# Kernel tuning notes

Measured on AMD Instinct MI355X. Metric: run time of the kernel, lower is better.

## Reference

```python
import jax, jax.numpy as jnp
import numpy as np

B, S, E, H, Dh, R, L = 32, 512, 512, 8, 64, 3, 2
NI, NS = 10000, 1000
SCALE = float(1.0 / np.sqrt(Dh))
NEG = -1000000000.0


def _tensor_attn(q, kv, Wq, bq, Wk, bk, Wv, bv, Wg, bg, Wtq, btq, Wtk, btk, core, mask):
    # q, kv: [B,S,E]
    Q = q @ Wq + bq
    K = kv @ Wk + bk
    V = kv @ Wv + bv
    # per-query global bias computed from full key projection: [B,S,H] -> [B,H,S,1]
    glo = jnp.transpose(K @ Wg + bg, (0, 2, 1))[..., None]
    Qh = Q.reshape(B, S, H, Dh).transpose(0, 2, 1, 3)  # [B,H,S,Dh]
    Kh = K.reshape(B, S, H, Dh).transpose(0, 2, 1, 3)
    Vh = V.reshape(B, S, H, Dh).transpose(0, 2, 1, 3)
    scores = jnp.einsum('bhqd,bhkd->bhqk', Qh, Kh)  # [B,H,S,S]
    # low-rank bilinear tensor-core term; note it depends only on position s
    qt = Qh @ Wtq + btq  # [B,H,S,R]
    kt = Kh @ Wtk + btk  # [B,H,S,R]
    ts = jnp.einsum('bhsi,ij,bhsj->bhs', qt, core, kt)  # [B,H,S]
    scores = (scores + glo + ts[..., None]) * SCALE
    scores = jnp.where(mask, NEG, scores)
    p = jax.nn.softmax(scores, axis=-1)
    out = jnp.einsum('bhqk,bhkd->bhqd', p, Vh)
    return out.transpose(0, 2, 1, 3).reshape(B, S, E)


def setup_inputs() -> dict:
    key = jax.random.key(0)
    ks = jax.random.split(key, 24)
    f = lambda k, shp, s=0.02: (jax.random.normal(k, shp, dtype=jnp.float32) * s)
    inp = {}
    inp['item_inputs'] = jax.random.randint(ks[0], (B, S), 0, NI)
    inp['skill_inputs'] = jax.random.randint(ks[1], (B, S), 0, NS)
    inp['label_inputs'] = jax.random.randint(ks[2], (B, S), 0, 2)
    inp['item_ids'] = jax.random.randint(ks[3], (B, S), 0, NI)
    inp['skill_ids'] = jax.random.randint(ks[4], (B, S), 0, NS)
    inp['item_emb'] = f(ks[5], (NI + 1, E // 2), 1.0).at[0].set(0.0)  # padding_idx=0
    inp['skill_emb'] = f(ks[6], (NS + 1, E // 2), 1.0).at[0].set(0.0)
    inp['W_in'] = f(ks[7], (2 * E, E))
    inp['b_in'] = jnp.zeros((E,), jnp.float32)
    inp['Wq'] = f(ks[8], (L, E, E))
    inp['bq'] = jnp.zeros((L, E), jnp.float32)
    inp['Wk'] = f(ks[9], (L, E, E))
    inp['bk'] = jnp.zeros((L, E), jnp.float32)
    inp['Wv'] = f(ks[10], (L, E, E))
    inp['bv'] = jnp.zeros((L, E), jnp.float32)
    inp['Wg'] = f(ks[11], (L, E, H))
    inp['bg'] = jnp.zeros((L, H), jnp.float32)
    inp['Wtq'] = f(ks[12], (L, Dh, R), 0.1)
    inp['btq'] = jnp.zeros((L, R), jnp.float32)
    inp['Wtk'] = f(ks[13], (L, Dh, R), 0.1)
    inp['btk'] = jnp.zeros((L, R), jnp.float32)
    inp['core'] = f(ks[14], (L, R, R), 0.5)
    inp['W_out'] = f(ks[15], (E, 1))
    inp['b_out'] = jnp.zeros((1,), jnp.float32)
    return inp


def reference(item_inputs, skill_inputs, label_inputs, item_ids, skill_ids,
              item_emb, skill_emb, W_in, b_in, Wq, bq, Wk, bk, Wv, bv,
              Wg, bg, Wtq, btq, Wtk, btk, core, W_out, b_out):
    # get_inputs
    ie = item_emb[item_inputs]    # [B,S,E/2]
    se = skill_emb[skill_inputs]
    lab = label_inputs[..., None].astype(jnp.float32)
    half = jnp.concatenate([ie, se], axis=-1)  # [B,S,E]
    inputs = jnp.concatenate([half * lab, half * (1.0 - lab)], axis=-1)  # [B,S,2E]
    x = jax.nn.relu(inputs @ W_in + b_in)  # [B,S,E]
    # query
    query = jnp.concatenate([item_emb[item_ids], skill_emb[skill_ids]], axis=-1)
    mask = jnp.triu(jnp.ones((1, 1, S, S), dtype=bool), k=1)
    out = _tensor_attn(query, x, Wq[0], bq[0], Wk[0], bk[0], Wv[0], bv[0],
                       Wg[0], bg[0], Wtq[0], btq[0], Wtk[0], btk[0], core[0], mask)
    for l in range(1, L):
        res = _tensor_attn(query, out, Wq[l], bq[l], Wk[l], bk[l], Wv[l], bv[l],
                           Wg[l], bg[l], Wtq[l], btq[l], Wtk[l], btk[l], core[l], mask)
        out = out + jax.nn.relu(res)
    return out @ W_out + b_out  # [B,S,1]
```

## Files before the change

kernel.cpp:

```cpp
#include <hip/hip_runtime.h>
#include <stdint.h>


typedef short short8v __attribute__((ext_vector_type(8)));
typedef float f32x4 __attribute__((ext_vector_type(4)));

__device__ __forceinline__ float bf2f(unsigned short u) {
  union { unsigned int i; float f; } c;
  c.i = ((unsigned int)u) << 16;
  return c.f;
}
__device__ __forceinline__ unsigned short f2bf(float f) {
  union { float f; unsigned int i; } c;
  c.f = f;
  unsigned int u = c.i + 0x7FFFu + ((c.i >> 16) & 1u);
  return (unsigned short)(u >> 16);
}

__device__ __forceinline__ void g2l16(const void* g, void* l) {
  __builtin_amdgcn_global_load_lds(
      (const __attribute__((address_space(1))) unsigned int*)g,
      (__attribute__((address_space(3))) unsigned int*)l, 16, 0, 0);
}

struct WPtrs {
  const float* s[7];
  unsigned short* d[7];
};
__global__ __launch_bounds__(256) void transpose_all_k(WPtrs p) {
  __shared__ float t[32][33];
  int by = blockIdx.y;
  int mi, r0t;
  if (by < 32) { mi = 0; r0t = by; }
  else { mi = 1 + ((by - 32) >> 4); r0t = (by - 32) & 15; }
  const float* in = p.s[mi];
  unsigned short* out = p.d[mi];
  int R = (mi == 0) ? 1024 : 512;
  const int C = 512;
  int c0 = blockIdx.x * 32, r0 = r0t * 32;
  int lr = threadIdx.x >> 5, lc = threadIdx.x & 31;
#pragma unroll
  for (int i = 0; i < 4; ++i) {
    int r = lr + i * 8;
    t[r][lc] = in[(size_t)(r0 + r) * C + (c0 + lc)];
  }
  __syncthreads();
#pragma unroll
  for (int i = 0; i < 4; ++i) {
    int r = lr + i * 8;
    out[(size_t)(c0 + r) * R + (r0 + lc)] = f2bf(t[lc][r]);
  }
}

__global__ __launch_bounds__(256) void build_inputs_k(
    const int* __restrict__ item_in, const int* __restrict__ skill_in,
    const int* __restrict__ label_in, const int* __restrict__ item_id,
    const int* __restrict__ skill_id, const float* __restrict__ iemb,
    const float* __restrict__ semb, unsigned short* __restrict__ INP,
    unsigned short* __restrict__ QRY) {
  int w = threadIdx.x >> 6, lane = threadIdx.x & 63;
  int row = blockIdx.x * 4 + w;
  int ii = item_in[row], si = skill_in[row], lb = label_in[row];
  int iq = item_id[row], sq = skill_id[row];
  int c = lane * 16;
  int k = c & 511;
  const float* src = (k < 256) ? (iemb + (size_t)ii * 256 + k)
                               : (semb + (size_t)si * 256 + (k - 256));
  bool keep = ((lb == 1) == (c < 512));
  union { unsigned short u[16]; int4 v[2]; } o;
#pragma unroll
  for (int i = 0; i < 16; ++i) o.u[i] = keep ? f2bf(src[i]) : 0;
  *(int4*)(INP + (size_t)row * 1024 + c) = o.v[0];
  *(int4*)(INP + (size_t)row * 1024 + c + 8) = o.v[1];
  int qc = lane * 8;
  const float* qs = (qc < 256) ? (iemb + (size_t)iq * 256 + qc)
                               : (semb + (size_t)sq * 256 + (qc - 256));
  union { unsigned short u[8]; int4 v; } q;
#pragma unroll
  for (int i = 0; i < 8; ++i) q.u[i] = f2bf(qs[i]);
  *(int4*)(QRY + (size_t)row * 512 + qc) = q.v;
}

#define CT_LD 132
template <int MT>
__global__ __launch_bounds__(256, 4) void gemm_bt_k(
    const unsigned short* __restrict__ A, const unsigned short* __restrict__ Bt,
    unsigned short* __restrict__ C, int K, int ldc,
    const float* __restrict__ biasA, const float* __restrict__ biasB,
    int nsplit, float scale, int do_relu) {
  constexpr int NT = (MT == 128) ? 4 : 2;
  constexpr int US = ((MT * 64 + 128 * 64) > (MT * 132)) ? (MT * 64 + 128 * 64) : (MT * 132);
  __shared__ __align__(16) unsigned short uS[US];
  unsigned short* sA = uS;
  unsigned short* sB = uS + MT * 64;
  unsigned short* Ct = uS;
  int mb = blockIdx.x, nb = blockIdx.y;
  int tid = threadIdx.x;
  int w = tid >> 6, lane = tid & 63, l16 = lane & 15, quad = lane >> 4;
  int wm = (MT == 128) ? (w & 1) : 0;
  int wn = (MT == 128) ? (w >> 1) : w;
  f32x4 acc[4][NT];
#pragma unroll
  for (int i = 0; i < 4; ++i)
#pragma unroll
    for (int jn = 0; jn < NT; ++jn) acc[i][jn] = (f32x4){0.f, 0.f, 0.f, 0.f};

  for (int k0 = 0; k0 < K; k0 += 64) {
    __syncthreads();
#pragma unroll
    for (int jj = 0; jj < MT / 32; ++jj) {
      int c = jj * 256 + tid;
      int row = c >> 3, kc = c & 7;
      int src = kc ^ (row & 7);
      g2l16(A + (size_t)(mb * MT + row) * K + k0 + src * 8, sA + (size_t)c * 8);
    }
#pragma unroll
    for (int jj = 0; jj < 4; ++jj) {
      int c = jj * 256 + tid;
      int row = c >> 3, kc = c & 7;
      int src = kc ^ (row & 7);
      g2l16(Bt + (size_t)(nb * 128 + row) * K + k0 + src * 8, sB + (size_t)c * 8);
    }
    __syncthreads();
#pragma unroll
    for (int kk = 0; kk < 2; ++kk) {
      short8v aF[4], bF[NT];
#pragma unroll
      for (int mt = 0; mt < 4; ++mt) {
        int r = wm * 64 + mt * 16 + l16;
        aF[mt] = *(const short8v*)(sA + r * 64 + (((kk * 4 + quad) ^ (r & 7)) << 3));
      }
#pragma unroll
      for (int nt = 0; nt < NT; ++nt) {
        int r = wn * (16 * NT) + nt * 16 + l16;
        bF[nt] = *(const short8v*)(sB + r * 64 + (((kk * 4 + quad) ^ (r & 7)) << 3));
      }
#pragma unroll
      for (int mt = 0; mt < 4; ++mt)
#pragma unroll
        for (int nt = 0; nt < NT; ++nt)
          acc[mt][nt] =
              __builtin_amdgcn_mfma_f32_16x16x32_bf16(aF[mt], bF[nt], acc[mt][nt], 0, 0, 0);
    }
  }
  __syncthreads();
#pragma unroll
  for (int mt = 0; mt < 4; ++mt)
#pragma unroll
    for (int nt = 0; nt < NT; ++nt) {
      int col = wn * (16 * NT) + nt * 16 + l16;
      int gcol = nb * 128 + col;
      float bs = (gcol < nsplit) ? biasA[gcol] : biasB[gcol - nsplit];
#pragma unroll
      for (int r = 0; r < 4; ++r) {
        int row = wm * 64 + mt * 16 + quad * 4 + r;
        float v = (acc[mt][nt][r] + bs) * scale;
        if (do_relu) v = fmaxf(v, 0.f);
        Ct[row * CT_LD + col] = f2bf(v);
      }
    }
  __syncthreads();
#pragma unroll
  for (int it = 0; it < MT / 16; ++it) {
    int row = it * 16 + (tid >> 4);
    int col8 = (tid & 15) * 8;
    *(int4*)(C + (size_t)(mb * MT + row) * ldc + nb * 128 + col8) =
        *(const int4*)(Ct + row * CT_LD + col8);
  }
}

#define VP_LD 264
__global__ __launch_bounds__(256) void vperm_k(const unsigned short* __restrict__ KVb,
                                               unsigned short* __restrict__ VT) {
  __shared__ __align__(16) unsigned short stg[64 * VP_LD];
  int kt = blockIdx.x, half = blockIdx.y, b = blockIdx.z;
  int t = threadIdx.x;
#pragma unroll
  for (int i = 0; i < 8; ++i) {
    int ch = i * 256 + t;
    int kp = ch >> 5, c = ch & 31;
    *(int4*)(stg + kp * VP_LD + c * 8) =
        *(const int4*)(KVb + (size_t)(b * 512 + kt * 64 + kp) * 1024 + 512 + half * 256 + c * 8);
  }
  __syncthreads();
#pragma unroll
  for (int i = 0; i < 8; ++i) {
    int ch = i * 256 + t;
    int d = ch >> 3, cc = ch & 7;
    union { unsigned short u[8]; int4 v; } o;
#pragma unroll
    for (int s = 0; s < 8; ++s) {
      int kp = ((cc >> 2) << 5) | ((s >> 2) << 4) | ((cc & 3) << 2) | (s & 3);
      o.u[s] = stg[kp * VP_LD + d];
    }
    *(int4*)(VT + (size_t)(b * 512 + half * 256 + d) * 512 + kt * 64 + cc * 8) = o.v;
  }
}

__global__ __launch_bounds__(256, 4) void attn_k(const unsigned short* __restrict__ Qb,
                                                 const unsigned short* __restrict__ KVb,
                                                 const unsigned short* __restrict__ VT,
                                                 unsigned short* __restrict__ Out) {
  __shared__ __align__(16) unsigned short sK[64 * 64];
  __shared__ __align__(16) unsigned short sV[64 * 64];
  int tid = threadIdx.x;
  int w = tid >> 6, lane = tid & 63;
  int l16 = lane & 15, quad = lane >> 4;
  int bh = blockIdx.x;
  int b = bh >> 3, h = bh & 7;
  int jb = 7 - (int)blockIdx.y;
  int qb = jb * 64 + w * 16;
  f32x4 zf = {0.f, 0.f, 0.f, 0.f};
  short8v onesF;
#pragma unroll
  for (int i = 0; i < 8; ++i) onesF[i] = (short)0x3F80;

  short8v qF[2];
#pragma unroll
  for (int hf = 0; hf < 2; ++hf)
    qF[hf] = *(const short8v*)(Qb + (size_t)(b * 512 + qb + l16) * 512 + h * 64 + hf * 32 +
                               quad * 8);

  f32x4 O[4], RS = zf;
#pragma unroll
  for (int dt = 0; dt < 4; ++dt) O[dt] = zf;

  const unsigned short* Kg = KVb + (size_t)(b * 512) * 1024 + h * 64;
  const unsigned short* Vg = VT + (size_t)(bh * 64) * 512;

  for (int kt = 0; kt <= jb; ++kt) {
    __syncthreads();
#pragma unroll
    for (int jj = 0; jj < 2; ++jj) {
      int c = jj * 256 + tid;
      int row = c >> 3, kc = c & 7, src = kc ^ (row & 7);
      g2l16(Kg + (size_t)(kt * 64 + row) * 1024 + src * 8, sK + c * 8);
    }
#pragma unroll
    for (int jj = 0; jj < 2; ++jj) {
      int c = jj * 256 + tid;
      int row = c >> 3, kc = c & 7, src = kc ^ (row & 7);
      g2l16(Vg + (size_t)row * 512 + kt * 64 + src * 8, sV + c * 8);
    }
    __syncthreads();
#pragma unroll
    for (int kp = 0; kp < 2; ++kp) {
      int kb32 = kt * 64 + kp * 32;
      if (kb32 > qb) continue;
      short8v kC[2][2], vC[4];
#pragma unroll
      for (int v = 0; v < 2; ++v) {
        int r = kp * 32 + v * 16 + l16;
#pragma unroll
        for (int hf = 0; hf < 2; ++hf)
          kC[v][hf] = *(const short8v*)(sK + r * 64 + (((hf * 4 + quad) ^ (r & 7)) << 3));
      }
#pragma unroll
      for (int dt = 0; dt < 4; ++dt) {
        int r = dt * 16 + l16;
        vC[dt] = *(const short8v*)(sV + r * 64 + (((kp * 4 + quad) ^ (r & 7)) << 3));
      }
      f32x4 S[2];
#pragma unroll
      for (int v = 0; v < 2; ++v) {
        f32x4 s0 = __builtin_amdgcn_mfma_f32_16x16x32_bf16(kC[v][0], qF[0], zf, 0, 0, 0);
        S[v] = __builtin_amdgcn_mfma_f32_16x16x32_bf16(kC[v][1], qF[1], s0, 0, 0, 0);
      }
      if (kb32 + 31 > qb) {
#pragma unroll
        for (int v = 0; v < 2; ++v)
#pragma unroll
          for (int r = 0; r < 4; ++r)
            if (kb32 + v * 16 + quad * 4 + r > qb + l16) S[v][r] = -1e30f;
      }
      union { unsigned int u32[4]; short8v v8; } pk;
#pragma unroll
      for (int i = 0; i < 4; ++i) {
        int v = i >> 1, r0 = (i & 1) * 2;
        float e0 = __expf(S[v][r0]);
        float e1 = __expf(S[v][r0 + 1]);
        pk.u32[i] = (__float_as_uint(e0) >> 16) | (__float_as_uint(e1) & 0xFFFF0000u);
      }
#pragma unroll
      for (int dt = 0; dt < 4; ++dt)
        O[dt] = __builtin_amdgcn_mfma_f32_16x16x32_bf16(pk.v8, vC[dt], O[dt], 0, 0, 0);
      RS = __builtin_amdgcn_mfma_f32_16x16x32_bf16(pk.v8, onesF, RS, 0, 0, 0);
    }
  }
  float lr[4];
#pragma unroll
  for (int r = 0; r < 4; ++r) lr[r] = 1.f / RS[r];
#pragma unroll
  for (int dt = 0; dt < 4; ++dt)
#pragma unroll
    for (int r = 0; r < 4; ++r)
      Out[(size_t)(b * 512 + qb + quad * 4 + r) * 512 + h * 64 + dt * 16 + l16] =
          f2bf(O[dt][r] * lr[r]);
}

__global__ __launch_bounds__(256) void final_k(const unsigned short* __restrict__ out0,
                                               const unsigned short* __restrict__ res1,
                                               const float* __restrict__ wout,
                                               const float* __restrict__ bout,
                                               float* __restrict__ dst) {
  int w = threadIdx.x >> 6, lane = threadIdx.x & 63;
  int row = blockIdx.x * 4 + w;
  const unsigned short* o = out0 + (size_t)row * 512 + lane * 8;
  const unsigned short* r = res1 + (size_t)row * 512 + lane * 8;
  const float* wv = wout + lane * 8;
  float acc = 0.f;
#pragma unroll
  for (int i = 0; i < 8; ++i) {
    float rv = bf2f(r[i]);
    acc += (bf2f(o[i]) + fmaxf(rv, 0.f)) * wv[i];
  }
#pragma unroll
  for (int off = 1; off <= 32; off <<= 1) acc += __shfl_xor(acc, off);
  if (lane == 0) dst[row] = acc + bout[0];
}

extern "C" void kernel_launch(void* const* d_in, const int* in_sizes, int n_in,
                              void* d_out, int out_size, void* d_ws, size_t ws_size,
                              hipStream_t stream) {
  (void)in_sizes; (void)n_in; (void)out_size; (void)ws_size;
  const int* item_inputs = (const int*)d_in[0];
  const int* skill_inputs = (const int*)d_in[1];
  const int* label_inputs = (const int*)d_in[2];
  const int* item_ids = (const int*)d_in[3];
  const int* skill_ids = (const int*)d_in[4];
  const float* item_emb = (const float*)d_in[5];
  const float* skill_emb = (const float*)d_in[6];
  const float* W_in = (const float*)d_in[7];
  const float* b_in = (const float*)d_in[8];
  const float* Wq = (const float*)d_in[9];
  const float* bq = (const float*)d_in[10];
  const float* Wk = (const float*)d_in[11];
  const float* bk = (const float*)d_in[12];
  const float* Wv = (const float*)d_in[13];
  const float* bv = (const float*)d_in[14];
  const float* W_out = (const float*)d_in[22];
  const float* b_out = (const float*)d_in[23];

  unsigned short* ws = (unsigned short*)d_ws;
  unsigned short* INP = ws;
  unsigned short* OUT0 = ws;
  unsigned short* RES1 = ws + (size_t)16384 * 512;
  unsigned short* QRY = ws + (size_t)16384 * 1024;
  unsigned short* X = QRY + (size_t)16384 * 512;
  unsigned short* VT = X;
  unsigned short* Qb = X + (size_t)16384 * 512;
  unsigned short* KVb = Qb + (size_t)16384 * 512;
  unsigned short* WInT = KVb + (size_t)16384 * 1024;
  unsigned short* WqT0 = WInT + 512 * 1024;
  unsigned short* WqT1 = WqT0 + 512 * 512;
  unsigned short* WkvT0 = WqT1 + 512 * 512;
  unsigned short* WkvT1 = WkvT0 + 1024 * 512;

  WPtrs p;
  p.s[0] = W_in;           p.d[0] = WInT;
  p.s[1] = Wq;             p.d[1] = WqT0;
  p.s[2] = Wq + 262144;    p.d[2] = WqT1;
  p.s[3] = Wk;             p.d[3] = WkvT0;
  p.s[4] = Wv;             p.d[4] = WkvT0 + 262144;
  p.s[5] = Wk + 262144;    p.d[5] = WkvT1;
  p.s[6] = Wv + 262144;    p.d[6] = WkvT1 + 262144;
  transpose_all_k<<<dim3(16, 128), 256, 0, stream>>>(p);

  build_inputs_k<<<4096, 256, 0, stream>>>(item_inputs, skill_inputs, label_inputs, item_ids,
                                           skill_ids, item_emb, skill_emb, INP, QRY);
  gemm_bt_k<64><<<dim3(256, 4), 256, 0, stream>>>(INP, WInT, X, 1024, 512, b_in, b_in,
                                                  1 << 30, 1.0f, 1);

  const float SC = 0.125f;
  gemm_bt_k<64><<<dim3(256, 4), 256, 0, stream>>>(QRY, WqT0, Qb, 512, 512, bq, bq, 1 << 30,
                                                  SC, 0);
  gemm_bt_k<128><<<dim3(128, 8), 256, 0, stream>>>(X, WkvT0, KVb, 512, 1024, bk, bv, 512,
                                                   1.0f, 0);
  vperm_k<<<dim3(8, 2, 32), 256, 0, stream>>>(KVb, VT);
  attn_k<<<dim3(256, 8), 256, 0, stream>>>(Qb, KVb, VT, OUT0);
  gemm_bt_k<64><<<dim3(256, 4), 256, 0, stream>>>(QRY, WqT1, Qb, 512, 512, bq + 512,
                                                  bq + 512, 1 << 30, SC, 0);
  gemm_bt_k<128><<<dim3(128, 8), 256, 0, stream>>>(OUT0, WkvT1, KVb, 512, 1024, bk + 512,
                                                   bv + 512, 512, 1.0f, 0);
  vperm_k<<<dim3(8, 2, 32), 256, 0, stream>>>(KVb, VT);
  attn_k<<<dim3(256, 8), 256, 0, stream>>>(Qb, KVb, VT, RES1);
  final_k<<<4096, 256, 0, stream>>>(OUT0, RES1, W_out, b_out, (float*)d_out);
}
```

Measured before the change: 311.4 us.

## Skip zero half of input GEMM via label partitioning, fuse V transpose and Q projections

Rows are partitioned by label using atomics into a compacted half-width input, so the input projection GEMM runs with K=512 instead of the zero-padded K=1024, and results are scattered back through a permutation. The V transpose is fused into the KV GEMM epilogue, which removes the separate vperm kernels. Both layers' Q projections are merged into one wider GEMM. This saves FLOPs and launches at the cost of atomics, a scattered epilogue, and a nondeterministic row order.

```diff
diff --git a/kernel.cpp b/kernel.cpp
--- a/kernel.cpp
+++ b/kernel.cpp
@@ -27,9 +27,15 @@
   const float* s[7];
   unsigned short* d[7];
 };
-__global__ __launch_bounds__(256) void transpose_all_k(WPtrs p) {
+__global__ __launch_bounds__(256) void transpose_all_k(WPtrs p, int* __restrict__ iperm,
+                                                       int* __restrict__ cnt) {
+  int by = blockIdx.y;
+  if (by == 0) {
+    int gid = blockIdx.x * 256 + threadIdx.x;
+    if (gid < 2) cnt[gid] = 0;
+    for (int i = gid; i < 16512; i += 4096) iperm[i] = 16384 + (i & 127);
+  }
   __shared__ float t[32][33];
-  int by = blockIdx.y;
   int mi, r0t;
   if (by < 32) { mi = 0; r0t = by; }
   else { mi = 1 + ((by - 32) >> 4); r0t = (by - 32) & 15; }
@@ -56,22 +62,25 @@
     const int* __restrict__ item_in, const int* __restrict__ skill_in,
     const int* __restrict__ label_in, const int* __restrict__ item_id,
     const int* __restrict__ skill_id, const float* __restrict__ iemb,
-    const float* __restrict__ semb, unsigned short* __restrict__ INP,
-    unsigned short* __restrict__ QRY) {
+    const float* __restrict__ semb, unsigned short* __restrict__ HALFC,
+    unsigned short* __restrict__ QRY, int* __restrict__ iperm, int* __restrict__ cnt) {
   int w = threadIdx.x >> 6, lane = threadIdx.x & 63;
   int row = blockIdx.x * 4 + w;
   int ii = item_in[row], si = skill_in[row], lb = label_in[row];
   int iq = item_id[row], sq = skill_id[row];
-  int c = lane * 16;
-  int k = c & 511;
-  const float* src = (k < 256) ? (iemb + (size_t)ii * 256 + k)
-                               : (semb + (size_t)si * 256 + (k - 256));
-  bool keep = ((lb == 1) == (c < 512));
-  union { unsigned short u[16]; int4 v[2]; } o;
-#pragma unroll
-  for (int i = 0; i < 16; ++i) o.u[i] = keep ? f2bf(src[i]) : 0;
-  *(int4*)(INP + (size_t)row * 1024 + c) = o.v[0];
-  *(int4*)(INP + (size_t)row * 1024 + c + 8) = o.v[1];
+  int pos = 0;
+  if (lane == 0) {
+    pos = lb ? atomicAdd(cnt, 1) : (16511 - atomicAdd(cnt + 1, 1));
+    iperm[pos] = row;
+  }
+  pos = __shfl(pos, 0);
+  int c = lane * 8;
+  const float* src = (c < 256) ? (iemb + (size_t)ii * 256 + c)
+                               : (semb + (size_t)si * 256 + (c - 256));
+  union { unsigned short u[8]; int4 v; } o;
+#pragma unroll
+  for (int i = 0; i < 8; ++i) o.u[i] = f2bf(src[i]);
+  *(int4*)(HALFC + (size_t)pos * 512 + c) = o.v;
   int qc = lane * 8;
   const float* qs = (qc < 256) ? (iemb + (size_t)iq * 256 + qc)
                                : (semb + (size_t)sq * 256 + (qc - 256));
@@ -82,12 +91,13 @@
 }
 
 #define CT_LD 132
+
 template <int MT>
 __global__ __launch_bounds__(256, 4) void gemm_bt_k(
     const unsigned short* __restrict__ A, const unsigned short* __restrict__ Bt,
     unsigned short* __restrict__ C, int K, int ldc,
     const float* __restrict__ biasA, const float* __restrict__ biasB,
-    int nsplit, float scale, int do_relu) {
+    int nsplit, float scale, int do_relu, unsigned short* __restrict__ VTout) {
   constexpr int NT = (MT == 128) ? 4 : 2;
   constexpr int US = ((MT * 64 + 128 * 64) > (MT * 132)) ? (MT * 64 + 128 * 64) : (MT * 132);
   __shared__ __align__(16) unsigned short uS[US];
@@ -160,44 +170,113 @@
       }
     }
   __syncthreads();
-#pragma unroll
-  for (int it = 0; it < MT / 16; ++it) {
+  if (VTout && nb >= 4) {
+    int bb = mb >> 2, kpb = (mb & 3) * 128;
+#pragma unroll
+    for (int it = 0; it < 8; ++it) {
+      int idx = it * 256 + tid;
+      int dloc = idx >> 4, rem = idx & 15;
+      union { unsigned short u[8]; int4 v; } o;
+#pragma unroll
+      for (int s = 0; s < 8; ++s) {
+        int r = 32 * (rem >> 2) + 16 * (s >> 2) + 4 * (rem & 3) + (s & 3);
+        o.u[s] = Ct[r * CT_LD + dloc];
+      }
+      *(int4*)(VTout + (size_t)(bb * 512 + (nb - 4) * 128 + dloc) * 512 + kpb + rem * 8) = o.v;
+    }
+  } else {
+#pragma unroll
+    for (int it = 0; it < MT / 16; ++it) {
+      int row = it * 16 + (tid >> 4);
+      int col8 = (tid & 15) * 8;
+      *(int4*)(C + (size_t)(mb * MT + row) * ldc + nb * 128 + col8) =
+          *(const int4*)(Ct + row * CT_LD + col8);
+    }
+  }
+}
+
+__global__ __launch_bounds__(256, 4) void gemm_in_k(
+    const unsigned short* __restrict__ A, const unsigned short* __restrict__ Bt,
+    unsigned short* __restrict__ C, const int* __restrict__ iperm,
+    const int* __restrict__ cnt, const float* __restrict__ bias) {
+  __shared__ __align__(16) unsigned short uS[64 * 64 + 128 * 64];
+  unsigned short* sA = uS;
+  unsigned short* sB = uS + 64 * 64;
+  unsigned short* Ct = uS;
+  int mb = blockIdx.x, nb = blockIdx.y;
+  int tid = threadIdx.x;
+  int w = tid >> 6, lane = tid & 63, l16 = lane & 15, quad = lane >> 4;
+  int n1 = *cnt;
+  int koff = (mb < ((n1 + 63) >> 6)) ? 0 : 512;
+  f32x4 acc[4][2];
+#pragma unroll
+  for (int i = 0; i < 4; ++i)
+#pragma unroll
+    for (int jn = 0; jn < 2; ++jn) acc[i][jn] = (f32x4){0.f, 0.f, 0.f, 0.f};
+
+  for (int k0 = 0; k0 < 512; k0 += 64) {
+    __syncthreads();
+#pragma unroll
+    for (int jj = 0; jj < 2; ++jj) {
+      int c = jj * 256 + tid;
+      int row = c >> 3, kc = c & 7;
+      int src = kc ^ (row & 7);
+      g2l16(A + (size_t)(mb * 64 + row) * 512 + k0 + src * 8, sA + (size_t)c * 8);
+    }
+#pragma unroll
+    for (int jj = 0; jj < 4; ++jj) {
+      int c = jj * 256 + tid;
+      int row = c >> 3, kc = c & 7;
+      int src = kc ^ (row & 7);
+      g2l16(Bt + (size_t)(nb * 128 + row) * 1024 + koff + k0 + src * 8, sB + (size_t)c * 8);
+    }
+    __syncthreads();
+#pragma unroll
+    for (int kk = 0; kk < 2; ++kk) {
+      short8v aF[4], bF[2];
+#pragma unroll
+      for (int mt = 0; mt < 4; ++mt) {
+        int r = mt * 16 + l16;
+        aF[mt] = *(const short8v*)(sA + r * 64 + (((kk * 4 + quad) ^ (r & 7)) << 3));
+      }
+#pragma unroll
+      for (int nt = 0; nt < 2; ++nt) {
+        int r = w * 32 + nt * 16 + l16;
+        bF[nt] = *(const short8v*)(sB + r * 64 + (((kk * 4 + quad) ^ (r & 7)) << 3));
+      }
+#pragma unroll
+      for (int mt = 0; mt < 4; ++mt)
+#pragma unroll
+        for (int nt = 0; nt < 2; ++nt)
+          acc[mt][nt] =
+              __builtin_amdgcn_mfma_f32_16x16x32_bf16(aF[mt], bF[nt], acc[mt][nt], 0, 0, 0);
+    }
+  }
+  __syncthreads();
+#pragma unroll
+  for (int mt = 0; mt < 4; ++mt)
+#pragma unroll
+    for (int nt = 0; nt < 2; ++nt) {
+      int col = w * 32 + nt * 16 + l16;
+      float bs = bias[nb * 128 + col];
+#pragma unroll
+      for (int r = 0; r < 4; ++r) {
+        int row = mt * 16 + quad * 4 + r;
+        Ct[row * CT_LD + col] = f2bf(fmaxf(acc[mt][nt][r] + bs, 0.f));
+      }
+    }
+  __syncthreads();
+#pragma unroll
+  for (int it = 0; it < 4; ++it) {
     int row = it * 16 + (tid >> 4);
+    int tgt = iperm[mb * 64 + row];
     int col8 = (tid & 15) * 8;
-    *(int4*)(C + (size_t)(mb * MT + row) * ldc + nb * 128 + col8) =
-        *(const int4*)(Ct + row * CT_LD + col8);
-  }
-}
-
-#define VP_LD 264
-__global__ __launch_bounds__(256) void vperm_k(const unsigned short* __restrict__ KVb,
-                                               unsigned short* __restrict__ VT) {
-  __shared__ __align__(16) unsigned short stg[64 * VP_LD];
-  int kt = blockIdx.x, half = blockIdx.y, b = blockIdx.z;
-  int t = threadIdx.x;
-#pragma unroll
-  for (int i = 0; i < 8; ++i) {
-    int ch = i * 256 + t;
-    int kp = ch >> 5, c = ch & 31;
-    *(int4*)(stg + kp * VP_LD + c * 8) =
-        *(const int4*)(KVb + (size_t)(b * 512 + kt * 64 + kp) * 1024 + 512 + half * 256 + c * 8);
-  }
-  __syncthreads();
-#pragma unroll
-  for (int i = 0; i < 8; ++i) {
-    int ch = i * 256 + t;
-    int d = ch >> 3, cc = ch & 7;
-    union { unsigned short u[8]; int4 v; } o;
-#pragma unroll
-    for (int s = 0; s < 8; ++s) {
-      int kp = ((cc >> 2) << 5) | ((s >> 2) << 4) | ((cc & 3) << 2) | (s & 3);
-      o.u[s] = stg[kp * VP_LD + d];
-    }
-    *(int4*)(VT + (size_t)(b * 512 + half * 256 + d) * 512 + kt * 64 + cc * 8) = o.v;
+    *(int4*)(C + (size_t)tgt * 512 + nb * 128 + col8) = *(const int4*)(Ct + row * CT_LD + col8);
   }
 }
 
 __global__ __launch_bounds__(256, 4) void attn_k(const unsigned short* __restrict__ Qb,
+                                                 int ldq,
                                                  const unsigned short* __restrict__ KVb,
                                                  const unsigned short* __restrict__ VT,
                                                  unsigned short* __restrict__ Out) {
@@ -218,7 +297,7 @@
   short8v qF[2];
 #pragma unroll
   for (int hf = 0; hf < 2; ++hf)
-    qF[hf] = *(const short8v*)(Qb + (size_t)(b * 512 + qb + l16) * 512 + h * 64 + hf * 32 +
+    qF[hf] = *(const short8v*)(Qb + (size_t)(b * 512 + qb + l16) * ldq + h * 64 + hf * 32 +
                                quad * 8);
 
   f32x4 O[4], RS = zf;
@@ -342,47 +421,44 @@
   const float* b_out = (const float*)d_in[23];
 
   unsigned short* ws = (unsigned short*)d_ws;
-  unsigned short* INP = ws;
+  unsigned short* HALFC = ws;
   unsigned short* OUT0 = ws;
-  unsigned short* RES1 = ws + (size_t)16384 * 512;
-  unsigned short* QRY = ws + (size_t)16384 * 1024;
+  unsigned short* RES1 = ws + (size_t)16512 * 512;
+  unsigned short* QRY = RES1 + (size_t)16384 * 512;
   unsigned short* X = QRY + (size_t)16384 * 512;
-  unsigned short* VT = X;
-  unsigned short* Qb = X + (size_t)16384 * 512;
-  unsigned short* KVb = Qb + (size_t)16384 * 512;
+  unsigned short* Qb = X + (size_t)16512 * 512;
+  unsigned short* KVb = Qb + (size_t)16384 * 1024;
   unsigned short* WInT = KVb + (size_t)16384 * 1024;
-  unsigned short* WqT0 = WInT + 512 * 1024;
-  unsigned short* WqT1 = WqT0 + 512 * 512;
-  unsigned short* WkvT0 = WqT1 + 512 * 512;
-  unsigned short* WkvT1 = WkvT0 + 1024 * 512;
+  unsigned short* WqTC = WInT + 512 * 1024;
+  unsigned short* WkvT0 = WqTC + (size_t)1024 * 512;
+  unsigned short* WkvT1 = WkvT0 + (size_t)1024 * 512;
+  unsigned short* VT = WkvT1 + (size_t)1024 * 512;
+  int* IPERM = (int*)(VT + (size_t)16384 * 512);
+  int* CNT = IPERM + 16512;
 
   WPtrs p;
   p.s[0] = W_in;           p.d[0] = WInT;
-  p.s[1] = Wq;             p.d[1] = WqT0;
-  p.s[2] = Wq + 262144;    p.d[2] = WqT1;
+  p.s[1] = Wq;             p.d[1] = WqTC;
+  p.s[2] = Wq + 262144;    p.d[2] = WqTC + 512 * 512;
   p.s[3] = Wk;             p.d[3] = WkvT0;
   p.s[4] = Wv;             p.d[4] = WkvT0 + 262144;
   p.s[5] = Wk + 262144;    p.d[5] = WkvT1;
   p.s[6] = Wv + 262144;    p.d[6] = WkvT1 + 262144;
-  transpose_all_k<<<dim3(16, 128), 256, 0, stream>>>(p);
+  transpose_all_k<<<dim3(16, 128), 256, 0, stream>>>(p, IPERM, CNT);
 
   build_inputs_k<<<4096, 256, 0, stream>>>(item_inputs, skill_inputs, label_inputs, item_ids,
-                                           skill_ids, item_emb, skill_emb, INP, QRY);
-  gemm_bt_k<64><<<dim3(256, 4), 256, 0, stream>>>(INP, WInT, X, 1024, 512, b_in, b_in,
-                                                  1 << 30, 1.0f, 1);
+                                           skill_ids, item_emb, skill_emb, HALFC, QRY, IPERM,
+                                           CNT);
+  gemm_in_k<<<dim3(258, 4), 256, 0, stream>>>(HALFC, WInT, X, IPERM, CNT, b_in);
 
   const float SC = 0.125f;
-  gemm_bt_k<64><<<dim3(256, 4), 256, 0, stream>>>(QRY, WqT0, Qb, 512, 512, bq, bq, 1 << 30,
-                                                  SC, 0);
+  gemm_bt_k<128><<<dim3(128, 8), 256, 0, stream>>>(QRY, WqTC, Qb, 512, 1024, bq, bq + 512,
+                                                   512, SC, 0, nullptr);
   gemm_bt_k<128><<<dim3(128, 8), 256, 0, stream>>>(X, WkvT0, KVb, 512, 1024, bk, bv, 512,
-                                                   1.0f, 0);
-  vperm_k<<<dim3(8, 2, 32), 256, 0, stream>>>(KVb, VT);
-  attn_k<<<dim3(256, 8), 256, 0, stream>>>(Qb, KVb, VT, OUT0);
-  gemm_bt_k<64><<<dim3(256, 4), 256, 0, stream>>>(QRY, WqT1, Qb, 512, 512, bq + 512,
-                                                  bq + 512, 1 << 30, SC, 0);
+                                                   1.0f, 0, VT);
+  attn_k<<<dim3(256, 8), 256, 0, stream>>>(Qb, 1024, KVb, VT, OUT0);
   gemm_bt_k<128><<<dim3(128, 8), 256, 0, stream>>>(OUT0, WkvT1, KVb, 512, 1024, bk + 512,
-                                                   bv + 512, 512, 1.0f, 0);
-  vperm_k<<<dim3(8, 2, 32), 256, 0, stream>>>(KVb, VT);
-  attn_k<<<dim3(256, 8), 256, 0, stream>>>(Qb, KVb, VT, RES1);
+                                                   bv + 512, 512, 1.0f, 0, VT);
+  attn_k<<<dim3(256, 8), 256, 0, stream>>>(Qb + 512, 1024, KVb, VT, RES1);
   final_k<<<4096, 256, 0, stream>>>(OUT0, RES1, W_out, b_out, (float*)d_out);
 }
```

Result: slower. 431.9 us (+38.7%).
